# Kernel tuning notes

Measured on AMD Instinct MI355X. Metric: run time of the kernel, lower is better.

The kernel has to match this reference:

```python
import jax, jax.numpy as jnp
import numpy as np
from jax import lax

EPS = 1e-5
DN = ('NCHW', 'OIHW', 'NCHW')


def ternarize(w):
    # Standard TWN-style ternarization: {-1, 0, +1} with threshold 0.7*mean|w|
    thr = 0.7 * jnp.mean(jnp.abs(w))
    return jnp.sign(w) * (jnp.abs(w) > thr).astype(w.dtype)


def conv(x, w, b=None):
    y = lax.conv_general_dilated(x, w, (1, 1), 'VALID', dimension_numbers=DN)
    if b is not None:
        y = y + b[None, :, None, None]
    return y


def bn(x, g, be, m, v):
    inv = g / jnp.sqrt(v + EPS)
    return x * inv[None, :, None, None] + (be - m * inv)[None, :, None, None]


def maxpool2(x):
    return lax.reduce_window(x, -jnp.inf, lax.max, (1, 1, 2, 2), (1, 1, 2, 2), 'VALID')


def setup_inputs() -> dict:
    key = jax.random.key(0)
    ks = jax.random.split(key, 21)
    d = {}
    d['x'] = jax.random.normal(ks[0], (8192, 1, 28, 28), jnp.float32)
    d['w1'] = ternarize(jax.random.normal(ks[1], (32, 1, 5, 5), jnp.float32))
    d['b1'] = jax.random.normal(ks[2], (32,), jnp.float32) * 0.1
    d['g1'] = jax.random.uniform(ks[3], (32,), jnp.float32, 0.5, 1.5)
    d['be1'] = jax.random.normal(ks[4], (32,), jnp.float32) * 0.1
    d['m1'] = jax.random.normal(ks[5], (32,), jnp.float32) * 0.1
    d['v1'] = jax.random.uniform(ks[6], (32,), jnp.float32, 0.5, 1.5)
    d['w2'] = ternarize(jax.random.normal(ks[7], (64, 32, 5, 5), jnp.float32))
    d['b2'] = jax.random.normal(ks[8], (64,), jnp.float32) * 0.1
    d['g2'] = jax.random.uniform(ks[9], (64,), jnp.float32, 0.5, 1.5)
    d['be2'] = jax.random.normal(ks[10], (64,), jnp.float32) * 0.1
    d['m2'] = jax.random.normal(ks[11], (64,), jnp.float32) * 0.1
    d['v2'] = jax.random.uniform(ks[12], (64,), jnp.float32, 0.5, 1.5)
    d['w3'] = ternarize(jax.random.normal(ks[13], (512, 1024, 1, 1), jnp.float32))
    d['b3'] = jax.random.normal(ks[14], (512,), jnp.float32) * 0.1
    d['g3'] = jax.random.uniform(ks[15], (512,), jnp.float32, 0.5, 1.5)
    d['be3'] = jax.random.normal(ks[16], (512,), jnp.float32) * 0.1
    d['m3'] = jax.random.normal(ks[17], (512,), jnp.float32) * 0.1
    d['v3'] = jax.random.uniform(ks[18], (512,), jnp.float32, 0.5, 1.5)
    d['w4'] = jax.random.normal(ks[19], (10, 512, 1, 1), jnp.float32) * 0.05
    return d


def reference(x, w1, b1, g1, be1, m1, v1, w2, b2, g2, be2, m2, v2,
              w3, b3, g3, be3, m3, v3, w4):
    h = conv(x, w1, b1)                       # [B,32,24,24]
    h = maxpool2(jax.nn.relu(bn(h, g1, be1, m1, v1)))   # [B,32,12,12]
    h = conv(h, w2, b2)                       # [B,64,8,8]
    h = maxpool2(jax.nn.relu(bn(h, g2, be2, m2, v2)))   # [B,64,4,4]
    h = h.reshape(-1, 1024, 1, 1)             # flatten C,H,W
    h = jax.nn.relu(bn(conv(h, w3, b3), g3, be3, m3, v3))  # [B,512,1,1]
    h = conv(h, w4)                            # [B,10,1,1]
    return h.reshape(-1, 10)
```

## Files before the change

kernel.cpp:

```cpp
#include <hip/hip_runtime.h>

#define EPS 1e-5f

typedef float f32x4 __attribute__((ext_vector_type(4)));
typedef short short8_t __attribute__((ext_vector_type(8)));
typedef unsigned int uint4v __attribute__((ext_vector_type(4)));
typedef unsigned short ushort_t;

__global__ void prep_kernel(const float* __restrict__ b1, const float* __restrict__ g1,
                            const float* __restrict__ be1, const float* __restrict__ m1,
                            const float* __restrict__ v1,
                            const float* __restrict__ b2, const float* __restrict__ g2,
                            const float* __restrict__ be2, const float* __restrict__ m2,
                            const float* __restrict__ v2,
                            const float* __restrict__ b3, const float* __restrict__ g3,
                            const float* __restrict__ be3, const float* __restrict__ m3,
                            const float* __restrict__ v3,
                            const float* __restrict__ w1, const float* __restrict__ w2,
                            const float* __restrict__ w3,
                            ushort_t* __restrict__ w1frag, ushort_t* __restrict__ w2frag,
                            ushort_t* __restrict__ w3frag, float* __restrict__ prm) {
  int tid = blockIdx.x * blockDim.x + threadIdx.x;
  int stride = gridDim.x * blockDim.x;
  for (int c = tid; c < 32; c += stride) {
    float s = g1[c] / sqrtf(v1[c] + EPS);
    prm[c] = s;
    prm[32 + c] = (b1[c] - m1[c]) * s + be1[c];
  }
  for (int c = tid; c < 64; c += stride) {
    float s = g2[c] / sqrtf(v2[c] + EPS);
    prm[64 + c] = s;
    prm[128 + c] = (b2[c] - m2[c]) * s + be2[c];
  }
  for (int c = tid; c < 512; c += stride) {
    float s = g3[c] / sqrtf(v3[c] + EPS);
    prm[192 + c] = s;
    prm[704 + c] = (b3[c] - m3[c]) * s + be3[c];
  }
  for (int i = tid; i < 2 * 2 * 64 * 8; i += stride) {
    const int j = i & 7;
    const int l = (i >> 3) & 63;
    const int nt = (i >> 9) & 1;
    const int p = i >> 10;
    const int oc = nt * 16 + (l & 15);
    const int t = (l >> 4) * 8 + j;
    const float v = (t < 25) ? w1[oc * 25 + t] : 0.f;
    const unsigned u = __float_as_uint(v);
    const ushort_t hi = (ushort_t)(u >> 16);
    const float r = v - __uint_as_float(u & 0xffff0000u);
    const ushort_t lo = (ushort_t)(__float_as_uint(r) >> 16);
    w1frag[i] = p ? lo : hi;
  }
  for (int i = tid; i < 25 * 4 * 64 * 8; i += stride) {
    const int kk = i >> 11;
    const int r = i & 2047;
    const int nt = r >> 9;
    const int r2 = r & 511;
    const int l = r2 >> 3;
    const int j = r2 & 7;
    const int oc = nt * 16 + (l & 15);
    const int ic = (l >> 4) * 8 + j;
    w2frag[i] = (ushort_t)(__float_as_uint(w2[oc * 800 + ic * 25 + kk]) >> 16);
  }
  for (int i = tid; i < 32 * 32 * 64 * 8; i += stride) {
    const int ks = i >> 14;
    const int r = i & 16383;
    const int ntg = r >> 9;
    const int r2 = r & 511;
    const int l = r2 >> 3;
    const int j = r2 & 7;
    const int oc = ntg * 16 + (l & 15);
    const int k = ks * 32 + (l >> 4) * 8 + j;
    w3frag[i] = (ushort_t)(__float_as_uint(w3[oc * 1024 + k]) >> 16);
  }
}

__launch_bounds__(128)
__global__ void conv12_kernel(const float* __restrict__ x,
                              const ushort_t* __restrict__ w1frag,
                              const ushort_t* __restrict__ w2frag,
                              const float* __restrict__ prm,
                              ushort_t* __restrict__ h2pH, ushort_t* __restrict__ h2pL) {
  __shared__ __align__(16) unsigned char lds[52480];

  const int tid = threadIdx.x;
  const int w = tid >> 6, l = tid & 63;
  const int b = blockIdx.x * 2 + w;
  const int m15 = l & 15, g = l >> 4;

  unsigned char* arena = lds + w * 26240;
  float* imgf = (float*)arena;
  ushort_t* insA = (ushort_t*)(arena + 3200);

  const float* xb = x + (size_t)b * 784;
#pragma unroll
  for (int it = 0; it < 4; ++it) {
    const int idx = it * 64 + l;
    if (idx < 196) ((float4*)imgf)[idx] = ((const float4*)xb)[idx];
  }
  if (l < 16) imgf[784 + l] = 0.f;

  short8_t B1h[2], B1l[2];
#pragma unroll
  for (int nt = 0; nt < 2; ++nt) {
    B1h[nt] = *(const short8_t*)(w1frag + (size_t)(nt * 64 + l) * 8);
    B1l[nt] = *(const short8_t*)(w1frag + (size_t)((2 + nt) * 64 + l) * 8);
  }

  int off[8];
#pragma unroll
  for (int j = 0; j < 8; ++j) {
    const int t = g * 8 + j;
    const int ky = t / 5, kx = t - ky * 5;
    off[j] = (t < 25) ? (ky * 28 + kx) : 0;
  }

  float s1[2], sh1[2], s2[4], sh2[4];
#pragma unroll
  for (int nt = 0; nt < 2; ++nt) {
    s1[nt] = prm[nt * 16 + m15];
    sh1[nt] = prm[32 + nt * 16 + m15];
  }
#pragma unroll
  for (int nt = 0; nt < 4; ++nt) {
    s2[nt] = prm[64 + nt * 16 + m15];
    sh2[nt] = prm[128 + nt * 16 + m15];
  }

#pragma unroll 1
  for (int mt = 0; mt < 36; ++mt) {
    const int q = mt * 16 + m15;
    const int p_pool = q >> 2, sub = q & 3;
    const int py = p_pool / 12, px = p_pool - py * 12;
    const int Y = 2 * py + (sub >> 1), X = 2 * px + (sub & 1);
    const float* pixb = imgf + Y * 28 + X;
    float v[8];
#pragma unroll
    for (int j = 0; j < 8; ++j) v[j] = pixb[off[j]];
    uint4v hv, lv;
#pragma unroll
    for (int k = 0; k < 4; ++k) {
      const unsigned u0 = __float_as_uint(v[2 * k]);
      const unsigned u1 = __float_as_uint(v[2 * k + 1]);
      hv[k] = (u0 >> 16) | (u1 & 0xffff0000u);
      const float r0 = v[2 * k] - __uint_as_float(u0 & 0xffff0000u);
      const float r1 = v[2 * k + 1] - __uint_as_float(u1 & 0xffff0000u);
      lv[k] = (__float_as_uint(r0) >> 16) | (__float_as_uint(r1) & 0xffff0000u);
    }
    const short8_t ah = __builtin_bit_cast(short8_t, hv);
    const short8_t al = __builtin_bit_cast(short8_t, lv);

    f32x4 c0 = {0.f, 0.f, 0.f, 0.f}, c1 = {0.f, 0.f, 0.f, 0.f};
    c0 = __builtin_amdgcn_mfma_f32_16x16x32_bf16(ah, B1h[0], c0, 0, 0, 0);
    c1 = __builtin_amdgcn_mfma_f32_16x16x32_bf16(ah, B1h[1], c1, 0, 0, 0);
    c0 = __builtin_amdgcn_mfma_f32_16x16x32_bf16(al, B1h[0], c0, 0, 0, 0);
    c1 = __builtin_amdgcn_mfma_f32_16x16x32_bf16(al, B1h[1], c1, 0, 0, 0);
    c0 = __builtin_amdgcn_mfma_f32_16x16x32_bf16(ah, B1l[0], c0, 0, 0, 0);
    c1 = __builtin_amdgcn_mfma_f32_16x16x32_bf16(ah, B1l[1], c1, 0, 0, 0);

    const int cell = mt * 4 + g;
#pragma unroll
    for (int nt = 0; nt < 2; ++nt) {
      const f32x4 c = nt ? c1 : c0;
      const float pv = fmaxf(fmaxf(c[0], c[1]), fmaxf(c[2], c[3]));
      const float a = fmaxf(fmaf(pv, s1[nt], sh1[nt]), 0.f);
      const unsigned u = __float_as_uint(a);
      const float r = a - __uint_as_float(u & 0xffff0000u);
      const int ic = nt * 16 + m15;
      insA[cell * 40 + ic] = (ushort_t)(u >> 16);
      insA[5760 + cell * 40 + ic] = (ushort_t)(__float_as_uint(r) >> 16);
    }
  }

  const int sy = (m15 & 3) >> 1, sx = m15 & 1;
  const int X2 = 2 * (m15 >> 2) + sx;

  f32x4 acc[4][4];
#pragma unroll
  for (int mt2 = 0; mt2 < 4; ++mt2)
#pragma unroll
    for (int nt = 0; nt < 4; ++nt) acc[mt2][nt] = (f32x4){0.f, 0.f, 0.f, 0.f};

#pragma unroll 1
  for (int pass = 0; pass < 5; ++pass) {
    short8_t wr[5][4];
#pragma unroll
    for (int kx = 0; kx < 5; ++kx)
#pragma unroll
      for (int nt = 0; nt < 4; ++nt)
        wr[kx][nt] = *(const short8_t*)(w2frag + (size_t)(((pass * 5 + kx) * 4 + nt) * 64 + l) * 8);
#pragma unroll
    for (int kx = 0; kx < 5; ++kx) {
#pragma unroll
      for (int mt2 = 0; mt2 < 4; ++mt2) {
        const int cellin = (2 * mt2 + sy + pass) * 12 + X2 + kx;
        const short8_t aH = *(const short8_t*)(insA + cellin * 40 + g * 8);
        const short8_t aL = *(const short8_t*)(insA + 5760 + cellin * 40 + g * 8);
#pragma unroll
        for (int nt = 0; nt < 4; ++nt) {
          acc[mt2][nt] = __builtin_amdgcn_mfma_f32_16x16x32_bf16(aH, wr[kx][nt], acc[mt2][nt], 0, 0, 0);
          acc[mt2][nt] = __builtin_amdgcn_mfma_f32_16x16x32_bf16(aL, wr[kx][nt], acc[mt2][nt], 0, 0, 0);
        }
      }
    }
  }

  const size_t ob = (size_t)b * 1024;
#pragma unroll
  for (int mt2 = 0; mt2 < 4; ++mt2) {
    const int cell2 = mt2 * 4 + g;
#pragma unroll
    for (int nt = 0; nt < 4; ++nt) {
      const f32x4 c = acc[mt2][nt];
      const float pv = fmaxf(fmaxf(c[0], c[1]), fmaxf(c[2], c[3]));
      const float a = fmaxf(fmaf(pv, s2[nt], sh2[nt]), 0.f);
      const unsigned u = __float_as_uint(a);
      const float r = a - __uint_as_float(u & 0xffff0000u);
      const int oc = nt * 16 + m15;
      h2pH[ob + oc * 16 + cell2] = (ushort_t)(u >> 16);
      h2pL[ob + oc * 16 + cell2] = (ushort_t)(__float_as_uint(r) >> 16);
    }
  }
}

__launch_bounds__(256)
__global__ void fc3_kernel(const ushort_t* __restrict__ h2pH, const ushort_t* __restrict__ h2pL,
                           const ushort_t* __restrict__ w3frag, const float* __restrict__ prm,
                           float* __restrict__ a3) {
  const int orig = blockIdx.x + (blockIdx.y << 3);
  const int xcd = orig & 7;
  const int j = orig >> 3;
  const int ytile = (xcd << 4) | (j >> 3);
  const int xtile = j & 7;
  const int n0 = xtile * 64;
  const int m0 = ytile * 64;
  const int w = threadIdx.x >> 6, l = threadIdx.x & 63;
  const int mrow = m0 + w * 16 + (l & 15);
  const int kc8 = (l >> 4) * 8;

  const ushort_t* aHp = h2pH + (size_t)mrow * 1024 + kc8;
  const ushort_t* aLp = h2pL + (size_t)mrow * 1024 + kc8;
  const ushort_t* bp = w3frag + (size_t)(n0 >> 4) * 512 + (size_t)l * 8;

  f32x4 accH[4], accL[4];
#pragma unroll
  for (int t = 0; t < 4; ++t) {
    accH[t] = (f32x4){0.f, 0.f, 0.f, 0.f};
    accL[t] = (f32x4){0.f, 0.f, 0.f, 0.f};
  }

#pragma unroll 2
  for (int ks = 0; ks < 32; ++ks) {
    const short8_t aH = *(const short8_t*)(aHp + ks * 32);
    const short8_t aL = *(const short8_t*)(aLp + ks * 32);
    const ushort_t* bks = bp + (size_t)ks * 16384;
#pragma unroll
    for (int t = 0; t < 4; ++t) {
      const short8_t bb = *(const short8_t*)(bks + t * 512);
      accH[t] = __builtin_amdgcn_mfma_f32_16x16x32_bf16(aH, bb, accH[t], 0, 0, 0);
      accL[t] = __builtin_amdgcn_mfma_f32_16x16x32_bf16(aL, bb, accL[t], 0, 0, 0);
    }
  }

#pragma unroll
  for (int t = 0; t < 4; ++t) {
    const int oc = n0 + t * 16 + (l & 15);
    const float s = prm[192 + oc], sh = prm[704 + oc];
#pragma unroll
    for (int r = 0; r < 4; ++r) {
      const int m = m0 + w * 16 + (l >> 4) * 4 + r;
      a3[(size_t)m * 512 + oc] = fmaxf(fmaf(accH[t][r] + accL[t][r], s, sh), 0.f);
    }
  }
}

__launch_bounds__(256)
__global__ void fc4_kernel(const float* __restrict__ a3, const float* __restrict__ w4,
                           float* __restrict__ out, int B) {
  const int w = threadIdx.x >> 6, l = threadIdx.x & 63;
  const int b = blockIdx.x * 4 + w;
  if (b >= B) return;
  const float4* ar = (const float4*)(a3 + (size_t)b * 512);
  const float4 a0 = ar[l * 2];
  const float4 a1 = ar[l * 2 + 1];
#pragma unroll
  for (int j = 0; j < 10; ++j) {
    const float4* wr = (const float4*)(w4 + j * 512);
    const float4 w0 = wr[l * 2];
    const float4 w1 = wr[l * 2 + 1];
    float sv = a0.x * w0.x + a0.y * w0.y + a0.z * w0.z + a0.w * w0.w +
               a1.x * w1.x + a1.y * w1.y + a1.z * w1.z + a1.w * w1.w;
#pragma unroll
    for (int off = 1; off < 64; off <<= 1) sv += __shfl_xor(sv, off);
    if (l == 0) out[(size_t)b * 10 + j] = sv;
  }
}

extern "C" void kernel_launch(void* const* d_in, const int* in_sizes, int n_in,
                              void* d_out, int out_size, void* d_ws, size_t ws_size,
                              hipStream_t stream) {
  const float* x  = (const float*)d_in[0];
  const float* w1 = (const float*)d_in[1];
  const float* b1 = (const float*)d_in[2];
  const float* g1 = (const float*)d_in[3];
  const float* be1 = (const float*)d_in[4];
  const float* m1 = (const float*)d_in[5];
  const float* v1 = (const float*)d_in[6];
  const float* w2 = (const float*)d_in[7];
  const float* b2 = (const float*)d_in[8];
  const float* g2 = (const float*)d_in[9];
  const float* be2 = (const float*)d_in[10];
  const float* m2 = (const float*)d_in[11];
  const float* v2 = (const float*)d_in[12];
  const float* w3 = (const float*)d_in[13];
  const float* b3 = (const float*)d_in[14];
  const float* g3 = (const float*)d_in[15];
  const float* be3 = (const float*)d_in[16];
  const float* m3 = (const float*)d_in[17];
  const float* v3 = (const float*)d_in[18];
  const float* w4 = (const float*)d_in[19];

  const int B = in_sizes[0] / 784;

  float* prm = (float*)d_ws;
  ushort_t* w1frag = (ushort_t*)(prm + 1216);
  ushort_t* w2frag = w1frag + 2048;
  ushort_t* w3frag = w2frag + 51200;
  ushort_t* h2pH = w3frag + 524288;
  ushort_t* h2pL = h2pH + (size_t)B * 1024;
  float* a3 = (float*)(h2pL + (size_t)B * 1024);

  prep_kernel<<<64, 256, 0, stream>>>(b1, g1, be1, m1, v1, b2, g2, be2, m2, v2,
                                      b3, g3, be3, m3, v3, w1, w2, w3,
                                      w1frag, w2frag, w3frag, prm);
  conv12_kernel<<<B / 2, 128, 0, stream>>>(x, w1frag, w2frag, prm, h2pH, h2pL);
  dim3 g3d(8, B / 64);
  fc3_kernel<<<g3d, 256, 0, stream>>>(h2pH, h2pL, w3frag, prm, a3);
  fc4_kernel<<<(B + 3) / 4, 256, 0, stream>>>(a3, w4, (float*)d_out, B);
}
```

Baseline: 320.1 us.

## Split each conv image across two waves instead of one wave per image

Each block now processes a single image using both waves: the conv1 M-tiles are split 18/18 between waves, and the conv2 output rows are split 2/2. Shared memory per block is halved and __syncthreads barriers are added between the stages. The intent is to double the number of blocks, halve per-wave latency and accumulator registers (allowing higher occupancy), at the cost of reloading w2 fragments per wave for half the work and adding barrier overhead.

```diff
diff --git a/kernel.cpp b/kernel.cpp
--- a/kernel.cpp
+++ b/kernel.cpp
@@ -81,24 +81,19 @@
                               const ushort_t* __restrict__ w2frag,
                               const float* __restrict__ prm,
                               ushort_t* __restrict__ h2pH, ushort_t* __restrict__ h2pL) {
-  __shared__ __align__(16) unsigned char lds[52480];
+  __shared__ __align__(16) unsigned char lds[26240];
 
   const int tid = threadIdx.x;
   const int w = tid >> 6, l = tid & 63;
-  const int b = blockIdx.x * 2 + w;
+  const int b = blockIdx.x;
   const int m15 = l & 15, g = l >> 4;
 
-  unsigned char* arena = lds + w * 26240;
-  float* imgf = (float*)arena;
-  ushort_t* insA = (ushort_t*)(arena + 3200);
+  float* imgf = (float*)lds;
+  ushort_t* insA = (ushort_t*)(lds + 3200);
 
   const float* xb = x + (size_t)b * 784;
-#pragma unroll
-  for (int it = 0; it < 4; ++it) {
-    const int idx = it * 64 + l;
-    if (idx < 196) ((float4*)imgf)[idx] = ((const float4*)xb)[idx];
-  }
-  if (l < 16) imgf[784 + l] = 0.f;
+  for (int i = tid; i < 196; i += 128) ((float4*)imgf)[i] = ((const float4*)xb)[i];
+  if (tid < 16) imgf[784 + tid] = 0.f;
 
   short8_t B1h[2], B1l[2];
 #pragma unroll
@@ -126,9 +121,11 @@
     s2[nt] = prm[64 + nt * 16 + m15];
     sh2[nt] = prm[128 + nt * 16 + m15];
   }
+  __syncthreads();
 
 #pragma unroll 1
-  for (int mt = 0; mt < 36; ++mt) {
+  for (int i = 0; i < 18; ++i) {
+    const int mt = w * 18 + i;
     const int q = mt * 16 + m15;
     const int p_pool = q >> 2, sub = q & 3;
     const int py = p_pool / 12, px = p_pool - py * 12;
@@ -171,15 +168,16 @@
       insA[5760 + cell * 40 + ic] = (ushort_t)(__float_as_uint(r) >> 16);
     }
   }
+  __syncthreads();
 
   const int sy = (m15 & 3) >> 1, sx = m15 & 1;
   const int X2 = 2 * (m15 >> 2) + sx;
 
-  f32x4 acc[4][4];
-#pragma unroll
-  for (int mt2 = 0; mt2 < 4; ++mt2)
-#pragma unroll
-    for (int nt = 0; nt < 4; ++nt) acc[mt2][nt] = (f32x4){0.f, 0.f, 0.f, 0.f};
+  f32x4 acc[2][4];
+#pragma unroll
+  for (int m = 0; m < 2; ++m)
+#pragma unroll
+    for (int nt = 0; nt < 4; ++nt) acc[m][nt] = (f32x4){0.f, 0.f, 0.f, 0.f};
 
 #pragma unroll 1
   for (int pass = 0; pass < 5; ++pass) {
@@ -192,14 +190,15 @@
 #pragma unroll
     for (int kx = 0; kx < 5; ++kx) {
 #pragma unroll
-      for (int mt2 = 0; mt2 < 4; ++mt2) {
+      for (int m = 0; m < 2; ++m) {
+        const int mt2 = 2 * w + m;
         const int cellin = (2 * mt2 + sy + pass) * 12 + X2 + kx;
         const short8_t aH = *(const short8_t*)(insA + cellin * 40 + g * 8);
         const short8_t aL = *(const short8_t*)(insA + 5760 + cellin * 40 + g * 8);
 #pragma unroll
         for (int nt = 0; nt < 4; ++nt) {
-          acc[mt2][nt] = __builtin_amdgcn_mfma_f32_16x16x32_bf16(aH, wr[kx][nt], acc[mt2][nt], 0, 0, 0);
-          acc[mt2][nt] = __builtin_amdgcn_mfma_f32_16x16x32_bf16(aL, wr[kx][nt], acc[mt2][nt], 0, 0, 0);
+          acc[m][nt] = __builtin_amdgcn_mfma_f32_16x16x32_bf16(aH, wr[kx][nt], acc[m][nt], 0, 0, 0);
+          acc[m][nt] = __builtin_amdgcn_mfma_f32_16x16x32_bf16(aL, wr[kx][nt], acc[m][nt], 0, 0, 0);
         }
       }
     }
@@ -207,11 +206,11 @@
 
   const size_t ob = (size_t)b * 1024;
 #pragma unroll
-  for (int mt2 = 0; mt2 < 4; ++mt2) {
-    const int cell2 = mt2 * 4 + g;
+  for (int m = 0; m < 2; ++m) {
+    const int cell2 = (2 * w + m) * 4 + g;
 #pragma unroll
     for (int nt = 0; nt < 4; ++nt) {
-      const f32x4 c = acc[mt2][nt];
+      const f32x4 c = acc[m][nt];
       const float pv = fmaxf(fmaxf(c[0], c[1]), fmaxf(c[2], c[3]));
       const float a = fmaxf(fmaf(pv, s2[nt], sh2[nt]), 0.f);
       const unsigned u = __float_as_uint(a);
@@ -333,7 +332,7 @@
   prep_kernel<<<64, 256, 0, stream>>>(b1, g1, be1, m1, v1, b2, g2, be2, m2, v2,
                                       b3, g3, be3, m3, v3, w1, w2, w3,
                                       w1frag, w2frag, w3frag, prm);
-  conv12_kernel<<<B / 2, 128, 0, stream>>>(x, w1frag, w2frag, prm, h2pH, h2pL);
+  conv12_kernel<<<B, 128, 0, stream>>>(x, w1frag, w2frag, prm, h2pH, h2pL);
   dim3 g3d(8, B / 64);
   fc3_kernel<<<g3d, 256, 0, stream>>>(h2pH, h2pL, w3frag, prm, a3);
   fc4_kernel<<<(B + 3) / 4, 256, 0, stream>>>(a3, w4, (float*)d_out, B);
```

Result: faster. 283.1 us (-11.6%).
